# Optimization experiments

Measured on AMD Instinct MI355X. Metric: run time of the kernel, lower is better.

Reference implementation:

```python
import jax, jax.numpy as jnp
import numpy as np

N_USERS = 50000
N_ENT = 100000
N_EDGES = 2_000_000
N_INTER = 1_000_000
CHANNEL = 64
N_HEADS = 2
D_K = CHANNEL // N_HEADS
N_HOPS = 2
N_REL = 10  # relation_emb has N_REL-1 rows


def setup_inputs() -> dict:
    key = jax.random.key(0)
    ks = jax.random.split(key, 8)
    user_emb = jax.random.normal(ks[0], (N_USERS, CHANNEL), jnp.float32) * 0.1
    entity_emb = jax.random.normal(ks[1], (N_ENT, CHANNEL), jnp.float32) * 0.1
    relation_emb = jax.random.normal(ks[2], (N_REL - 1, CHANNEL), jnp.float32) * 0.1
    W_Q = jax.random.normal(ks[3], (CHANNEL, CHANNEL), jnp.float32) * (1.0 / np.sqrt(CHANNEL))
    edge_index = jax.random.randint(ks[4], (2, N_EDGES), 0, N_ENT)
    edge_type = jax.random.randint(ks[5], (N_EDGES,), 1, N_REL)  # in [1, N_REL-1]
    inter_edge = jnp.stack([
        jax.random.randint(ks[6], (N_INTER,), 0, N_USERS),
        jax.random.randint(ks[7], (N_INTER,), 0, N_ENT),
    ])
    inter_edge_w = jnp.full((N_INTER,), 1.0 / 20.0, jnp.float32)
    return {
        "user_emb": user_emb,
        "entity_emb": entity_emb,
        "relation_emb": relation_emb,
        "W_Q": W_Q,
        "inter_edge_w": inter_edge_w,
        "edge_index": edge_index,
        "edge_type": edge_type,
        "inter_edge": inter_edge,
    }


def _l2norm(x):
    # F.normalize(dim=-1) with eps=1e-12
    n = jnp.linalg.norm(x, axis=-1, keepdims=True)
    return x / jnp.maximum(n, 1e-12)


def _scatter_softmax(logits, seg, num_segments):
    # per-segment (over leading axis) numerically-stable softmax; logits [E, H]
    m = jax.ops.segment_max(logits, seg, num_segments=num_segments)
    e = jnp.exp(logits - m[seg])
    s = jax.ops.segment_sum(e, seg, num_segments=num_segments)
    return e / s[seg]


def reference(user_emb, entity_emb, relation_emb, W_Q, inter_edge_w,
              edge_index, edge_type, inter_edge):
    head, tail = edge_index[0], edge_index[1]
    u_idx, i_idx = inter_edge[0], inter_edge[1]
    rel = relation_emb[edge_type - 1]  # [E, C]
    inv_sqrt_dk = 1.0 / np.sqrt(D_K)

    entity_res, user_res = entity_emb, user_emb
    for _ in range(N_HOPS):
        h_emb = entity_emb[head]                       # [E, C]
        t_emb = entity_emb[tail]                       # [E, C]
        q = (h_emb @ W_Q).reshape(-1, N_HEADS, D_K)    # [E, H, Dk]
        k = (t_emb @ W_Q).reshape(-1, N_HEADS, D_K) * rel.reshape(-1, N_HEADS, D_K)
        score = (q * k).sum(-1) * inv_sqrt_dk          # [E, H]
        attn = _scatter_softmax(score, head, N_ENT)    # [E, H]
        value = (t_emb * rel).reshape(-1, N_HEADS, D_K)
        agg = (value * attn[..., None]).reshape(-1, CHANNEL)
        entity_agg = jax.ops.segment_sum(agg, head, num_segments=N_ENT)
        item_agg = inter_edge_w[:, None] * entity_emb[i_idx]
        user_agg = jax.ops.segment_sum(item_agg, u_idx, num_segments=N_USERS)
        # mess_dropout disabled (eval mode)
        entity_emb = _l2norm(entity_agg)
        user_emb = _l2norm(user_agg)
        entity_res = entity_res + entity_emb
        user_res = user_res + user_emb
    return entity_res, user_res
```

## Files before the change

kernel.cpp:

```cpp
#include <hip/hip_runtime.h>

#define NU     50000
#define NEN    100000
#define NEDGE  2000000
#define NINTER 1000000
#define CH     64
#define NRELM1 9
#define CAPE   64
#define CAPU   64

#define BINSH   8
#define NBINE   ((NEN + 255) >> BINSH)
#define NBINU   ((NU  + 255) >> BINSH)
#define CAPBE   6144
#define CAPBU   6144
#define CHUNK   8192
#define NBE_BLK ((NEDGE  + CHUNK - 1) / CHUNK)
#define NBU_BLK ((NINTER + CHUNK - 1) / CHUNK)
#define NSTR_E  ((NEN * CH) / 2048)
#define NSTR_U  ((NU * CH + 2047) / 2048)

typedef _Float16 hv2 __attribute__((ext_vector_type(2)));
typedef _Float16 h8  __attribute__((ext_vector_type(8)));
typedef float    f32x4 __attribute__((ext_vector_type(4)));
union P4 { float4 f; hv2 h[4]; };

__global__ __launch_bounds__(256) void k_bin(
    const float* __restrict__ ue, const float* __restrict__ ee,
    const float* __restrict__ re, const float* __restrict__ wq,
    const float* __restrict__ iw, const int* __restrict__ eidx,
    const int* __restrict__ etype, const int* __restrict__ ii,
    _Float16* __restrict__ Eh, float* __restrict__ Eres, float* __restrict__ Ures,
    _Float16* __restrict__ Relh, _Float16* __restrict__ Wt,
    int* __restrict__ binCurE, int* __restrict__ binCurU,
    int* __restrict__ binBufE, unsigned long long* __restrict__ binBufU)
{
    __shared__ int hist[NBINE];
    __shared__ int gbase[NBINE];
    int b = blockIdx.x, tid = threadIdx.x;

    if (b < NBE_BLK) {
        for (int i = tid; i < NBINE; i += 256) hist[i] = 0;
        __syncthreads();
        int base = b * CHUNK;
        int n = NEDGE - base; if (n > CHUNK) n = CHUNK;
        for (int i = tid; i < n; i += 256)
            atomicAdd(&hist[eidx[base + i] >> BINSH], 1);
        __syncthreads();
        for (int i = tid; i < NBINE; i += 256) {
            int c = hist[i];
            gbase[i] = c ? atomicAdd(&binCurE[i], c) : 0;
            hist[i] = 0;
        }
        __syncthreads();
        for (int i = tid; i < n; i += 256) {
            int h  = eidx[base + i];
            int t  = eidx[NEDGE + base + i];
            int rt = etype[base + i] - 1;
            int bin = h >> BINSH;
            int pos = atomicAdd(&hist[bin], 1);
            int g = gbase[bin] + pos;
            if (g < CAPBE)
                __hip_atomic_store(&binBufE[bin * CAPBE + g],
                                   (h & 255) | ((t | (rt << 17)) << 8),
                                   __ATOMIC_RELAXED, __HIP_MEMORY_SCOPE_AGENT);
        }
    } else if (b < NBE_BLK + NBU_BLK) {
        for (int i = tid; i < NBINU; i += 256) hist[i] = 0;
        __syncthreads();
        int base = (b - NBE_BLK) * CHUNK;
        int n = NINTER - base; if (n > CHUNK) n = CHUNK;
        for (int i = tid; i < n; i += 256)
            atomicAdd(&hist[ii[base + i] >> BINSH], 1);
        __syncthreads();
        for (int i = tid; i < NBINU; i += 256) {
            int c = hist[i];
            gbase[i] = c ? atomicAdd(&binCurU[i], c) : 0;
            hist[i] = 0;
        }
        __syncthreads();
        for (int i = tid; i < n; i += 256) {
            int u = ii[base + i];
            int e = ii[NINTER + base + i];
            unsigned w = __float_as_uint(iw[base + i]);
            int bin = u >> BINSH;
            int pos = atomicAdd(&hist[bin], 1);
            int g = gbase[bin] + pos;
            if (g < CAPBU)
                __hip_atomic_store(&binBufU[bin * CAPBU + g],
                                   (unsigned long long)((u & 255) | (e << 8))
                                 | ((unsigned long long)w << 32),
                                   __ATOMIC_RELAXED, __HIP_MEMORY_SCOPE_AGENT);
        }
    } else {
        int sb = b - (NBE_BLK + NBU_BLK);
        if (sb < NSTR_E) {
            int i0 = sb * 2048 + tid * 8;
            float4 a = *(const float4*)(ee + i0);
            float4 c = *(const float4*)(ee + i0 + 4);
            *(float4*)(Eres + i0)     = a;
            *(float4*)(Eres + i0 + 4) = c;
            P4 o;
            o.h[0].x = (_Float16)a.x; o.h[0].y = (_Float16)a.y;
            o.h[1].x = (_Float16)a.z; o.h[1].y = (_Float16)a.w;
            o.h[2].x = (_Float16)c.x; o.h[2].y = (_Float16)c.y;
            o.h[3].x = (_Float16)c.z; o.h[3].y = (_Float16)c.w;
            *(float4*)(Eh + i0) = o.f;
        } else if (sb < NSTR_E + NSTR_U) {
            int i0 = (sb - NSTR_E) * 2048 + tid * 8;
            if (i0 < NU * CH) {
                *(float4*)(Ures + i0)     = *(const float4*)(ue + i0);
                *(float4*)(Ures + i0 + 4) = *(const float4*)(ue + i0 + 4);
            }
        } else {
            for (int i = tid; i < NRELM1 * CH; i += 256)
                Relh[i] = (_Float16)re[i];
            for (int i = tid; i < CH * CH; i += 256)
                Wt[(i & 63) * 64 + (i >> 6)] = (_Float16)wq[i];
        }
    }
}

__global__ __launch_bounds__(256) void k_place(
    const int* __restrict__ binCurE, const int* __restrict__ binBufE,
    const int* __restrict__ binCurU, const unsigned long long* __restrict__ binBufU,
    int* __restrict__ cntE, int* __restrict__ csrE,
    int* __restrict__ cntU, unsigned long long* __restrict__ csrU2)
{
    __shared__ int cnt[256];
    int b = blockIdx.x, tid = threadIdx.x;
    cnt[tid] = 0;
    __syncthreads();
    if (b < NBINE) {
        int n = binCurE[b]; if (n > CAPBE) n = CAPBE;
        const int* buf = binBufE + b * CAPBE;
        for (int i = tid; i < n; i += 256) {
            int rec = buf[i];
            int nl = rec & 255;
            int pos = atomicAdd(&cnt[nl], 1);
            if (pos < CAPE) csrE[((b << BINSH) + nl) * CAPE + pos] = rec >> 8;
        }
        __syncthreads();
        int node = (b << BINSH) + tid;
        if (node < NEN) { int c = cnt[tid]; cntE[node] = c > CAPE ? CAPE : c; }
    } else {
        int ub = b - NBINE;
        int n = binCurU[ub]; if (n > CAPBU) n = CAPBU;
        const unsigned long long* buf = binBufU + ub * CAPBU;
        for (int i = tid; i < n; i += 256) {
            unsigned long long rec = buf[i];
            int nl = (int)rec & 255;
            int pos = atomicAdd(&cnt[nl], 1);
            if (pos < CAPU)
                csrU2[((ub << BINSH) + nl) * CAPU + pos] =
                    ((rec & 0xFFFFFFFFull) >> 8) | (rec & 0xFFFFFFFF00000000ull);
        }
        __syncthreads();
        int node = (ub << BINSH) + tid;
        if (node < NU) { int c = cnt[tid]; cntU[node] = c > CAPU ? CAPU : c; }
    }
}

__global__ __launch_bounds__(256) void k_gemm(
    const _Float16* __restrict__ Eh, const _Float16* __restrict__ Wt,
    _Float16* __restrict__ Qh)
{
    int w = threadIdx.x >> 6, lane = threadIdx.x & 63;
    int r0 = blockIdx.x * 64 + w * 16;
    if (r0 >= NEN) return;
    int lr = lane & 15, lg = lane >> 4;
    const _Float16* arow = Eh + (size_t)(r0 + lr) * 64 + lg * 8;
    h8 a0 = *(const h8*)(arow);
    h8 a1 = *(const h8*)(arow + 32);
#pragma unroll
    for (int ct = 0; ct < 4; ++ct) {
        const _Float16* brow = Wt + (ct * 16 + lr) * 64 + lg * 8;
        h8 b0 = *(const h8*)(brow);
        h8 b1 = *(const h8*)(brow + 32);
        f32x4 c = {0.f, 0.f, 0.f, 0.f};
        c = __builtin_amdgcn_mfma_f32_16x16x32_f16(a0, b0, c, 0, 0, 0);
        c = __builtin_amdgcn_mfma_f32_16x16x32_f16(a1, b1, c, 0, 0, 0);
#pragma unroll
        for (int r = 0; r < 4; ++r)
            Qh[(size_t)(r0 + lg * 4 + r) * 64 + ct * 16 + lr] = (_Float16)c[r];
    }
}

__global__ __launch_bounds__(256) void k_fused(
    const int* __restrict__ cntE, const int* __restrict__ csrE,
    const _Float16* __restrict__ Qh, const _Float16* __restrict__ Eh,
    const _Float16* __restrict__ Relh,
    _Float16* __restrict__ Ehn, float* __restrict__ Eres,
    const int* __restrict__ cntU, const unsigned long long* __restrict__ csrU2,
    float* __restrict__ Ures)
{
    int wid  = blockIdx.x * 4 + (threadIdx.x >> 6);
    int lane = threadIdx.x & 63;
    int s = lane >> 3, l = lane & 7;
    int c8 = l * 8;

    if (wid < NEN) {
        int row = wid;
        int cnt = cntE[row];
        int beg = row * CAPE, end = beg + cnt;
        P4 q; q.f = *(const float4*)(Qh + (size_t)row * 64 + c8);
        float acc[8] = {0.f,0.f,0.f,0.f,0.f,0.f,0.f,0.f};
        float den = 0.f;
        int a0 = beg + s;
        int pA = (a0 < end) ? csrE[a0] : 0;
        int pB = (a0 + 8 < end) ? csrE[a0 + 8] : 0;
        P4 ktA, teA, rlA;
        {
            int tail = pA & 0x1FFFF, rt = pA >> 17;
            ktA.f = *(const float4*)(Qh   + (size_t)tail * 64 + c8);
            teA.f = *(const float4*)(Eh   + (size_t)tail * 64 + c8);
            rlA.f = *(const float4*)(Relh + rt * 64 + c8);
        }
        int nit = (cnt + 7) >> 3;
        for (int it = 0; it < nit; ++it) {
            P4 ktB, teB, rlB;
            int tailB = pB & 0x1FFFF, rtB = pB >> 17;
            ktB.f = *(const float4*)(Qh   + (size_t)tailB * 64 + c8);
            teB.f = *(const float4*)(Eh   + (size_t)tailB * 64 + c8);
            rlB.f = *(const float4*)(Relh + rtB * 64 + c8);
            int a2 = beg + (it + 2) * 8 + s;
            int pN = (a2 < end) ? csrE[a2] : 0;
            bool act = (beg + it * 8 + s) < end;
            float sc = 0.f;
#pragma unroll
            for (int i = 0; i < 4; ++i) {
                hv2 km = ktA.h[i] * rlA.h[i];
                sc = __builtin_amdgcn_fdot2(q.h[i], km, sc, false);
            }
            sc += __shfl_xor(sc, 1);
            sc += __shfl_xor(sc, 2);
            float ex = act ? __expf(sc * 0.17677669529663687f) : 0.f;
            den += ex;
#pragma unroll
            for (int i = 0; i < 4; ++i) {
                hv2 vm = teA.h[i] * rlA.h[i];
                acc[2*i]   += ex * (float)vm.x;
                acc[2*i+1] += ex * (float)vm.y;
            }
            ktA = ktB; teA = teB; rlA = rlB; pB = pN;
        }
#pragma unroll
        for (int k = 0; k < 8; ++k) {
            acc[k] += __shfl_xor(acc[k], 8);
            acc[k] += __shfl_xor(acc[k], 16);
            acc[k] += __shfl_xor(acc[k], 32);
        }
        den += __shfl_xor(den, 8); den += __shfl_xor(den, 16); den += __shfl_xor(den, 32);
        float invd = (den > 0.f) ? 1.f / den : 0.f;
        float ss = 0.f;
#pragma unroll
        for (int k = 0; k < 8; ++k) { acc[k] *= invd; ss += acc[k] * acc[k]; }
        ss += __shfl_xor(ss, 1); ss += __shfl_xor(ss, 2); ss += __shfl_xor(ss, 4);
        float inv = 1.f / fmaxf(sqrtf(ss), 1e-12f);
#pragma unroll
        for (int k = 0; k < 8; ++k) acc[k] *= inv;
        if (s == 0) {
            P4 o;
#pragma unroll
            for (int i = 0; i < 4; ++i) { o.h[i].x = (_Float16)acc[2*i]; o.h[i].y = (_Float16)acc[2*i+1]; }
            *(float4*)(Ehn + (size_t)row * 64 + c8) = o.f;
            float4 r0 = *(const float4*)(Eres + (size_t)row * 64 + c8);
            float4 r1 = *(const float4*)(Eres + (size_t)row * 64 + c8 + 4);
            r0.x += acc[0]; r0.y += acc[1]; r0.z += acc[2]; r0.w += acc[3];
            r1.x += acc[4]; r1.y += acc[5]; r1.z += acc[6]; r1.w += acc[7];
            *(float4*)(Eres + (size_t)row * 64 + c8)     = r0;
            *(float4*)(Eres + (size_t)row * 64 + c8 + 4) = r1;
        }
    } else {
        int row = wid - NEN;
        int cnt = cntU[row];
        int beg = row * CAPU, end = beg + cnt;
        float acc[8] = {0.f,0.f,0.f,0.f,0.f,0.f,0.f,0.f};
        int a0 = beg + s;
        unsigned long long recA = (a0 < end) ? csrU2[a0] : 0ull;
        unsigned long long recB = (a0 + 8 < end) ? csrU2[a0 + 8] : 0ull;
        P4 teA; teA.f = *(const float4*)(Eh + (size_t)(unsigned)recA * 64 + c8);
        int nit = (cnt + 7) >> 3;
        for (int it = 0; it < nit; ++it) {
            P4 teB; teB.f = *(const float4*)(Eh + (size_t)(unsigned)recB * 64 + c8);
            int a2 = beg + (it + 2) * 8 + s;
            unsigned long long recN = (a2 < end) ? csrU2[a2] : 0ull;
            float wgt = __uint_as_float((unsigned)(recA >> 32));
#pragma unroll
            for (int i = 0; i < 4; ++i) {
                acc[2*i]   += wgt * (float)teA.h[i].x;
                acc[2*i+1] += wgt * (float)teA.h[i].y;
            }
            teA = teB; recA = recB; recB = recN;
        }
#pragma unroll
        for (int k = 0; k < 8; ++k) {
            acc[k] += __shfl_xor(acc[k], 8);
            acc[k] += __shfl_xor(acc[k], 16);
            acc[k] += __shfl_xor(acc[k], 32);
        }
        float ss = 0.f;
#pragma unroll
        for (int k = 0; k < 8; ++k) ss += acc[k] * acc[k];
        ss += __shfl_xor(ss, 1); ss += __shfl_xor(ss, 2); ss += __shfl_xor(ss, 4);
        float inv = 1.f / fmaxf(sqrtf(ss), 1e-12f);
        if (s == 0) {
            float4 r0 = *(const float4*)(Ures + (size_t)row * 64 + c8);
            float4 r1 = *(const float4*)(Ures + (size_t)row * 64 + c8 + 4);
            r0.x += acc[0] * inv; r0.y += acc[1] * inv; r0.z += acc[2] * inv; r0.w += acc[3] * inv;
            r1.x += acc[4] * inv; r1.y += acc[5] * inv; r1.z += acc[6] * inv; r1.w += acc[7] * inv;
            *(float4*)(Ures + (size_t)row * 64 + c8)     = r0;
            *(float4*)(Ures + (size_t)row * 64 + c8 + 4) = r1;
        }
    }
}

extern "C" void kernel_launch(void* const* d_in, const int* in_sizes, int n_in,
                              void* d_out, int out_size, void* d_ws, size_t ws_size,
                              hipStream_t stream)
{
    const float* ue = (const float*)d_in[0];
    const float* ee = (const float*)d_in[1];
    const float* re = (const float*)d_in[2];
    const float* wq = (const float*)d_in[3];
    const float* iw = (const float*)d_in[4];
    const int* eidx  = (const int*)d_in[5];
    const int* etype = (const int*)d_in[6];
    const int* ii    = (const int*)d_in[7];

    float* Eres = (float*)d_out;
    float* Ures = Eres + (size_t)NEN * CH;

    _Float16* Relh = (_Float16*)d_ws;
    _Float16* Wt   = Relh + 1024;
    _Float16* Qh   = Wt + 4096;
    _Float16* EhA  = Qh  + (size_t)NEN * CH;
    _Float16* EhB  = EhA + (size_t)NEN * CH;
    int* cntE      = (int*)(EhB + (size_t)NEN * CH);
    int* cntU      = cntE + NEN;
    int* csrE      = cntU + NU;
    unsigned long long* csrU2 = (unsigned long long*)(csrE + (size_t)NEN * CAPE);
    int* binCurE   = (int*)(csrU2 + (size_t)NU * CAPU);
    int* binCurU   = binCurE + NBINE;
    int* binBufE   = (int*)Qh;
    unsigned long long* binBufU = (unsigned long long*)EhB;

    hipMemsetAsync(binCurE, 0, (NBINE + NBINU) * sizeof(int), stream);
    k_bin<<<NBE_BLK + NBU_BLK + NSTR_E + NSTR_U + 1, 256, 0, stream>>>(
        ue, ee, re, wq, iw, eidx, etype, ii,
        EhA, Eres, Ures, Relh, Wt, binCurE, binCurU, binBufE, binBufU);
    k_place<<<NBINE + NBINU, 256, 0, stream>>>(binCurE, binBufE, binCurU, binBufU,
                                               cntE, csrE, cntU, csrU2);

    _Float16* Ehc = EhA;
    _Float16* Ehn = EhB;
    for (int hop = 0; hop < 2; ++hop) {
        k_gemm <<<(NEN + 63) / 64, 256, 0, stream>>>(Ehc, Wt, Qh);
        k_fused<<<(NEN + NU) / 4, 256, 0, stream>>>(cntE, csrE, Qh, Ehc, Relh,
                                                    Ehn, Eres, cntU, csrU2, Ures);
        _Float16* tmp = Ehc; Ehc = Ehn; Ehn = tmp;
    }
}
```

Measured before the change: 471.8 us.

## Replace global atomic bin cursors with per-block local sort and offset directory

The binning pass now sorts each input chunk by bin inside shared memory using a block-wide prefix scan, writes the sorted chunk contiguously, and records each bin's offset and count in a per-block directory. The placement kernel then has one thread per source block walk its slice of the directory. This removes the global atomic cursors, the memset and the scattered per-record global stores, and also the per-bin capacity limit that could drop records. In exchange it adds a scan with many barriers per block and a serial per-thread read loop in the placement kernel.

After: 433.7 us. 1.09x faster.

```diff
diff --git a/kernel.cpp b/kernel.cpp
--- a/kernel.cpp
+++ b/kernel.cpp
@@ -12,11 +12,12 @@
 #define BINSH   8
 #define NBINE   ((NEN + 255) >> BINSH)
 #define NBINU   ((NU  + 255) >> BINSH)
-#define CAPBE   6144
-#define CAPBU   6144
-#define CHUNK   8192
-#define NBE_BLK ((NEDGE  + CHUNK - 1) / CHUNK)
-#define NBU_BLK ((NINTER + CHUNK - 1) / CHUNK)
+#define CHUNKE  8192
+#define CHUNKU  4096
+#define NBE_BLK ((NEDGE  + CHUNKE - 1) / CHUNKE)
+#define NBU_BLK ((NINTER + CHUNKU - 1) / CHUNKU)
+#define DSTRE   416
+#define DSTRU   224
 #define NSTR_E  ((NEN * CH) / 2048)
 #define NSTR_U  ((NU * CH + 2047) / 2048)
 
@@ -32,66 +33,85 @@
     const int* __restrict__ etype, const int* __restrict__ ii,
     _Float16* __restrict__ Eh, float* __restrict__ Eres, float* __restrict__ Ures,
     _Float16* __restrict__ Relh, _Float16* __restrict__ Wt,
-    int* __restrict__ binCurE, int* __restrict__ binCurU,
-    int* __restrict__ binBufE, unsigned long long* __restrict__ binBufU)
-{
-    __shared__ int hist[NBINE];
-    __shared__ int gbase[NBINE];
+    unsigned* __restrict__ dirE, unsigned* __restrict__ dirU,
+    int* __restrict__ blkBufE, unsigned long long* __restrict__ blkBufU)
+{
+    __shared__ long long srt64[CHUNKU];
+    __shared__ int hist[512];
+    __shared__ int sc[512];
+    int* srt = (int*)srt64;
     int b = blockIdx.x, tid = threadIdx.x;
 
     if (b < NBE_BLK) {
-        for (int i = tid; i < NBINE; i += 256) hist[i] = 0;
-        __syncthreads();
-        int base = b * CHUNK;
-        int n = NEDGE - base; if (n > CHUNK) n = CHUNK;
+        hist[tid] = 0; hist[tid + 256] = 0;
+        __syncthreads();
+        int base = b * CHUNKE;
+        int n = NEDGE - base; if (n > CHUNKE) n = CHUNKE;
         for (int i = tid; i < n; i += 256)
             atomicAdd(&hist[eidx[base + i] >> BINSH], 1);
         __syncthreads();
-        for (int i = tid; i < NBINE; i += 256) {
-            int c = hist[i];
-            gbase[i] = c ? atomicAdd(&binCurE[i], c) : 0;
-            hist[i] = 0;
-        }
+        sc[tid] = hist[tid]; sc[tid + 256] = hist[tid + 256];
+        __syncthreads();
+#pragma unroll
+        for (int off = 1; off < 512; off <<= 1) {
+            int v0 = (tid >= off) ? sc[tid - off] : 0;
+            int v1 = sc[tid + 256 - off];
+            __syncthreads();
+            sc[tid] += v0; sc[tid + 256] += v1;
+            __syncthreads();
+        }
+        sc[tid] -= hist[tid]; sc[tid + 256] -= hist[tid + 256];
         __syncthreads();
         for (int i = tid; i < n; i += 256) {
             int h  = eidx[base + i];
             int t  = eidx[NEDGE + base + i];
             int rt = etype[base + i] - 1;
-            int bin = h >> BINSH;
-            int pos = atomicAdd(&hist[bin], 1);
-            int g = gbase[bin] + pos;
-            if (g < CAPBE)
-                __hip_atomic_store(&binBufE[bin * CAPBE + g],
-                                   (h & 255) | ((t | (rt << 17)) << 8),
-                                   __ATOMIC_RELAXED, __HIP_MEMORY_SCOPE_AGENT);
-        }
+            int pos = atomicAdd(&sc[h >> BINSH], 1);
+            srt[pos] = (h & 255) | ((t | (rt << 17)) << 8);
+        }
+        __syncthreads();
+        int4* dst = (int4*)(blkBufE + b * CHUNKE);
+        const int4* s4 = (const int4*)srt;
+        for (int j = tid; j < ((n + 3) >> 2); j += 256) dst[j] = s4[j];
+        for (int bin = tid; bin < NBINE; bin += 256)
+            dirE[b * DSTRE + bin] =
+                ((unsigned)(sc[bin] - hist[bin]) << 16) | (unsigned)hist[bin];
     } else if (b < NBE_BLK + NBU_BLK) {
-        for (int i = tid; i < NBINU; i += 256) hist[i] = 0;
-        __syncthreads();
-        int base = (b - NBE_BLK) * CHUNK;
-        int n = NINTER - base; if (n > CHUNK) n = CHUNK;
+        hist[tid] = 0; hist[tid + 256] = 0;
+        __syncthreads();
+        int ub = b - NBE_BLK;
+        int base = ub * CHUNKU;
+        int n = NINTER - base; if (n > CHUNKU) n = CHUNKU;
         for (int i = tid; i < n; i += 256)
             atomicAdd(&hist[ii[base + i] >> BINSH], 1);
         __syncthreads();
-        for (int i = tid; i < NBINU; i += 256) {
-            int c = hist[i];
-            gbase[i] = c ? atomicAdd(&binCurU[i], c) : 0;
-            hist[i] = 0;
-        }
+        sc[tid] = hist[tid]; sc[tid + 256] = hist[tid + 256];
+        __syncthreads();
+#pragma unroll
+        for (int off = 1; off < 512; off <<= 1) {
+            int v0 = (tid >= off) ? sc[tid - off] : 0;
+            int v1 = sc[tid + 256 - off];
+            __syncthreads();
+            sc[tid] += v0; sc[tid + 256] += v1;
+            __syncthreads();
+        }
+        sc[tid] -= hist[tid]; sc[tid + 256] -= hist[tid + 256];
         __syncthreads();
         for (int i = tid; i < n; i += 256) {
             int u = ii[base + i];
             int e = ii[NINTER + base + i];
             unsigned w = __float_as_uint(iw[base + i]);
-            int bin = u >> BINSH;
-            int pos = atomicAdd(&hist[bin], 1);
-            int g = gbase[bin] + pos;
-            if (g < CAPBU)
-                __hip_atomic_store(&binBufU[bin * CAPBU + g],
-                                   (unsigned long long)((u & 255) | (e << 8))
-                                 | ((unsigned long long)w << 32),
-                                   __ATOMIC_RELAXED, __HIP_MEMORY_SCOPE_AGENT);
-        }
+            int pos = atomicAdd(&sc[u >> BINSH], 1);
+            srt64[pos] = (unsigned long long)((u & 255) | (e << 8))
+                       | ((unsigned long long)w << 32);
+        }
+        __syncthreads();
+        int4* dst = (int4*)(blkBufU + (size_t)ub * CHUNKU);
+        const int4* s4 = (const int4*)srt64;
+        for (int j = tid; j < ((n + 1) >> 1); j += 256) dst[j] = s4[j];
+        for (int bin = tid; bin < NBINU; bin += 256)
+            dirU[ub * DSTRU + bin] =
+                ((unsigned)(sc[bin] - hist[bin]) << 16) | (unsigned)hist[bin];
     } else {
         int sb = b - (NBE_BLK + NBU_BLK);
         if (sb < NSTR_E) {
@@ -122,8 +142,8 @@
 }
 
 __global__ __launch_bounds__(256) void k_place(
-    const int* __restrict__ binCurE, const int* __restrict__ binBufE,
-    const int* __restrict__ binCurU, const unsigned long long* __restrict__ binBufU,
+    const unsigned* __restrict__ dirE, const int* __restrict__ blkBufE,
+    const unsigned* __restrict__ dirU, const unsigned long long* __restrict__ blkBufU,
     int* __restrict__ cntE, int* __restrict__ csrE,
     int* __restrict__ cntU, unsigned long long* __restrict__ csrU2)
 {
@@ -132,28 +152,34 @@
     cnt[tid] = 0;
     __syncthreads();
     if (b < NBINE) {
-        int n = binCurE[b]; if (n > CAPBE) n = CAPBE;
-        const int* buf = binBufE + b * CAPBE;
-        for (int i = tid; i < n; i += 256) {
-            int rec = buf[i];
-            int nl = rec & 255;
-            int pos = atomicAdd(&cnt[nl], 1);
-            if (pos < CAPE) csrE[((b << BINSH) + nl) * CAPE + pos] = rec >> 8;
+        if (tid < NBE_BLK) {
+            unsigned d = dirE[tid * DSTRE + b];
+            int off = d >> 16, c = d & 0xFFFF;
+            const int* src = blkBufE + tid * CHUNKE + off;
+            for (int i = 0; i < c; ++i) {
+                int rec = src[i];
+                int nl = rec & 255;
+                int pos = atomicAdd(&cnt[nl], 1);
+                if (pos < CAPE) csrE[((b << BINSH) + nl) * CAPE + pos] = rec >> 8;
+            }
         }
         __syncthreads();
         int node = (b << BINSH) + tid;
         if (node < NEN) { int c = cnt[tid]; cntE[node] = c > CAPE ? CAPE : c; }
     } else {
         int ub = b - NBINE;
-        int n = binCurU[ub]; if (n > CAPBU) n = CAPBU;
-        const unsigned long long* buf = binBufU + ub * CAPBU;
-        for (int i = tid; i < n; i += 256) {
-            unsigned long long rec = buf[i];
-            int nl = (int)rec & 255;
-            int pos = atomicAdd(&cnt[nl], 1);
-            if (pos < CAPU)
-                csrU2[((ub << BINSH) + nl) * CAPU + pos] =
-                    ((rec & 0xFFFFFFFFull) >> 8) | (rec & 0xFFFFFFFF00000000ull);
+        if (tid < NBU_BLK) {
+            unsigned d = dirU[tid * DSTRU + ub];
+            int off = d >> 16, c = d & 0xFFFF;
+            const unsigned long long* src = blkBufU + (size_t)tid * CHUNKU + off;
+            for (int i = 0; i < c; ++i) {
+                unsigned long long rec = src[i];
+                int nl = (int)rec & 255;
+                int pos = atomicAdd(&cnt[nl], 1);
+                if (pos < CAPU)
+                    csrU2[((ub << BINSH) + nl) * CAPU + pos] =
+                        ((rec & 0xFFFFFFFFull) >> 8) | (rec & 0xFFFFFFFF00000000ull);
+            }
         }
         __syncthreads();
         int node = (ub << BINSH) + tid;
@@ -340,16 +366,15 @@
     int* cntU      = cntE + NEN;
     int* csrE      = cntU + NU;
     unsigned long long* csrU2 = (unsigned long long*)(csrE + (size_t)NEN * CAPE);
-    int* binCurE   = (int*)(csrU2 + (size_t)NU * CAPU);
-    int* binCurU   = binCurE + NBINE;
-    int* binBufE   = (int*)Qh;
-    unsigned long long* binBufU = (unsigned long long*)EhB;
-
-    hipMemsetAsync(binCurE, 0, (NBINE + NBINU) * sizeof(int), stream);
+    unsigned* dirE = (unsigned*)(csrU2 + (size_t)NU * CAPU);
+    unsigned* dirU = dirE + NBE_BLK * DSTRE;
+    int* blkBufE   = (int*)Qh;
+    unsigned long long* blkBufU = (unsigned long long*)EhB;
+
     k_bin<<<NBE_BLK + NBU_BLK + NSTR_E + NSTR_U + 1, 256, 0, stream>>>(
         ue, ee, re, wq, iw, eidx, etype, ii,
-        EhA, Eres, Ures, Relh, Wt, binCurE, binCurU, binBufE, binBufU);
-    k_place<<<NBINE + NBINU, 256, 0, stream>>>(binCurE, binBufE, binCurU, binBufU,
+        EhA, Eres, Ures, Relh, Wt, dirE, dirU, blkBufE, blkBufU);
+    k_place<<<NBINE + NBINU, 256, 0, stream>>>(dirE, blkBufE, dirU, blkBufU,
                                                cntE, csrE, cntU, csrU2);
 
     _Float16* Ehc = EhA;
```
